# Kernel tuning notes

Hardware: AMD Instinct MI355X
Metric: run time of the kernel (lower is better)

The kernel has to match this reference:

```python
import jax, jax.numpy as jnp
import numpy as np

N_HEADS, D_MODEL, D_HEAD, N_CTX = 16, 2048, 128, 2048
BATCH, SEQ = 2, 2048
ATTN_SCALE = float(np.sqrt(D_HEAD))
IGNORE = -100000.0


def setup_inputs() -> dict:
    key = jax.random.key(0)
    ks = jax.random.split(key, 6)
    init = 0.02
    return {
        "residual": jax.random.normal(ks[0], (BATCH, SEQ, D_MODEL), dtype=jnp.float32),
        "x": jax.random.normal(ks[1], (BATCH, SEQ, D_MODEL), dtype=jnp.float32),
        "W_Q": jax.random.normal(ks[2], (N_HEADS, D_MODEL, D_HEAD), dtype=jnp.float32) * init,
        "W_K": jax.random.normal(ks[3], (N_HEADS, D_MODEL, D_HEAD), dtype=jnp.float32) * init,
        "W_V": jax.random.normal(ks[4], (N_HEADS, D_MODEL, D_HEAD), dtype=jnp.float32) * init,
        "W_O": jax.random.normal(ks[5], (N_HEADS, D_HEAD, D_MODEL), dtype=jnp.float32) * init,
        "b_Q": jnp.zeros((N_HEADS, D_HEAD), dtype=jnp.float32),
        "b_K": jnp.zeros((N_HEADS, D_HEAD), dtype=jnp.float32),
        "b_V": jnp.zeros((N_HEADS, D_HEAD), dtype=jnp.float32),
        "b_O": jnp.zeros((D_MODEL,), dtype=jnp.float32),
    }


def reference(residual, x, W_Q, W_K, W_V, W_O, b_Q, b_K, b_V, b_O):
    # use_split_qkv_input=False: QKV all read from residual
    q = jnp.einsum('bpm,hmd->bphd', residual, W_Q) + b_Q  # [b, pos, h, d_head]
    k = jnp.einsum('bpm,hmd->bphd', residual, W_K) + b_K
    v = jnp.einsum('bpm,hmd->bphd', residual, W_V) + b_V
    attn_scores = jnp.einsum('bqhd,bkhd->bhqk', q, k) / ATTN_SCALE  # [b, h, q, k]
    key_len = attn_scores.shape[-1]
    mask = jnp.tril(jnp.ones((key_len, key_len), dtype=bool))  # causal mask [q, k]
    attn_scores = jnp.where(mask, attn_scores, IGNORE)
    pattern = jax.nn.softmax(attn_scores, axis=-1)
    z = jnp.einsum('bkhd,bhqk->bqhd', v, pattern)
    out = jnp.einsum('bphd,hdm->bpm', z, W_O) + b_O
    return (residual, out)
```

## Files before the change

### kernel.cpp

```cpp
#include <hip/hip_runtime.h>
#include <hip/hip_bf16.h>

typedef __attribute__((ext_vector_type(8))) short bf16x8;
typedef __attribute__((ext_vector_type(4))) float f32x4;

#define N_HEADS 16
#define D_MODEL 2048
#define D_HEAD  128
#define SEQ     2048
#define BATCH   2
#define HD      (N_HEADS * D_HEAD)
#define QSCALE  0.08838834764831845f

__device__ inline __hip_bfloat16 to_bf16(float v) { return __float2bfloat16(v); }
__device__ inline __hip_bfloat16 to_bf16(__hip_bfloat16 v) { return v; }

typedef __attribute__((address_space(3))) unsigned lds_u32_t;
typedef __attribute__((address_space(1))) unsigned glb_u32_t;
__device__ inline void async16(void* l, const void* g) {
    __builtin_amdgcn_global_load_lds((const glb_u32_t*)g, (lds_u32_t*)l, 16, 0, 0);
}

__global__ __launch_bounds__(256) void cvt_dual(
    const float4* __restrict__ in, float4* __restrict__ o32,
    __hip_bfloat16* __restrict__ obf, long n4)
{
    for (long i = (long)blockIdx.x * blockDim.x + threadIdx.x; i < n4;
         i += (long)gridDim.x * blockDim.x) {
        float4 v = in[i];
        o32[i] = v;
        union { __hip_bfloat16 b[4]; uint2 u; } p;
        p.b[0] = __float2bfloat16(v.x);
        p.b[1] = __float2bfloat16(v.y);
        p.b[2] = __float2bfloat16(v.z);
        p.b[3] = __float2bfloat16(v.w);
        *(uint2*)(obf + 4 * i) = p.u;
    }
}

template <typename Tin>
__global__ __launch_bounds__(256) void transpose_to_bf16(
    const Tin* __restrict__ in, __hip_bfloat16* __restrict__ out,
    int R, int C, long in_rs, long in_bs, long out_bs)
{
    __shared__ Tin tile[64][65];
    const Tin* src = in + (long)blockIdx.z * in_bs;
    __hip_bfloat16* dst = out + (long)blockIdx.z * out_bs;
    const int c0 = blockIdx.x * 64, r0 = blockIdx.y * 64;
    const int t = threadIdx.x;
    const int tr = t >> 4;
    const int tc = (t & 15) * 4;
#pragma unroll
    for (int i = 0; i < 4; i++) {
        int r = tr + i * 16;
#pragma unroll
        for (int j = 0; j < 4; j++)
            tile[r][tc + j] = src[(long)(r0 + r) * in_rs + c0 + tc + j];
    }
    __syncthreads();
#pragma unroll
    for (int i = 0; i < 4; i++) {
        int c = tr + i * 16;
#pragma unroll
        for (int j = 0; j < 4; j++)
            dst[(long)(c0 + c) * R + r0 + tc + j] = to_bf16(tile[tc + j][c]);
    }
}

__device__ inline void store_out(__hip_bfloat16* p, float v) { *p = __float2bfloat16(v); }
__device__ inline void store_out(float* p, float v) { *p = v; }

template <typename OutT>
__global__ __launch_bounds__(256) void gemm_qkv(
    const __hip_bfloat16* __restrict__ A,
    const __hip_bfloat16* __restrict__ WTbase,
    const float* __restrict__ bQ, const float* bK, const float* bV,
    OutT* __restrict__ Cbase,
    int M, int N, int K, long wstride, long cstride, float scale0)
{
    __shared__ __align__(16) __hip_bfloat16 As[128 * 32];
    __shared__ __align__(16) __hip_bfloat16 Bs[128 * 32];
    const int z = blockIdx.z;
    const __hip_bfloat16* Bt = WTbase + (long)z * wstride;
    const float* bias = (z == 0) ? bQ : ((z == 1) ? bK : bV);
    OutT* C = Cbase + (long)z * cstride;
    const float outscale = (z == 0) ? scale0 : 1.0f;

    const int tid = threadIdx.x;
    const int lane = tid & 63, wave = tid >> 6;
    const int l15 = lane & 15, quad = lane >> 4;
    const int wr = wave >> 1, wc = wave & 1;
    const int m0 = blockIdx.y * 128, n0 = blockIdx.x * 128;

    const short* Ap = (const short*)A;
    const short* Bp = (const short*)Bt;

    f32x4 acc[4][4] = {};

    for (int k0 = 0; k0 < K; k0 += 32) {
        __syncthreads();
#pragma unroll
        for (int i = 0; i < 2; i++) {
            int e = i * 256 + tid;
            int row = e >> 2, ch = e & 3;
            async16((char*)As + (i * 256 + wave * 64) * 16,
                    Ap + (long)(m0 + row) * K + k0 + ch * 8);
            async16((char*)Bs + (i * 256 + wave * 64) * 16,
                    Bp + (long)(n0 + row) * K + k0 + ch * 8);
        }
        __syncthreads();

        bf16x8 af[4], bfr[4];
#pragma unroll
        for (int t = 0; t < 4; t++) {
            af[t]  = *(const bf16x8*)((const short*)As + (wr * 64 + t * 16 + l15) * 32 + quad * 8);
            bfr[t] = *(const bf16x8*)((const short*)Bs + (wc * 64 + t * 16 + l15) * 32 + quad * 8);
        }
#pragma unroll
        for (int i = 0; i < 4; i++)
#pragma unroll
            for (int j = 0; j < 4; j++)
                acc[i][j] = __builtin_amdgcn_mfma_f32_16x16x32_bf16(af[i], bfr[j], acc[i][j], 0, 0, 0);
    }

    const int mw = m0 + wr * 64, nw = n0 + wc * 64;
#pragma unroll
    for (int i = 0; i < 4; i++) {
#pragma unroll
        for (int j = 0; j < 4; j++) {
            int n = nw + j * 16 + l15;
            float bv = bias[n];
#pragma unroll
            for (int r = 0; r < 4; r++) {
                int m = mw + i * 16 + quad * 4 + r;
                store_out(&C[(long)m * N + n], (acc[i][j][r] + bv) * outscale);
            }
        }
    }
}

template <typename OutT>
__global__ __launch_bounds__(512, 2) void gemm256(
    const __hip_bfloat16* __restrict__ A,
    const __hip_bfloat16* __restrict__ WTbase,
    const float* __restrict__ bQ, const float* bK, const float* bV,
    OutT* __restrict__ Cbase,
    int N, int K, long wstride, long cstride, float scale0,
    int nx, int ny)
{
    __shared__ __align__(16) short lds[2][4][128 * 64];

    const int tid = threadIdx.x;
    const int lane = tid & 63;
    const int wave = tid >> 6;
    const int l15 = lane & 15, quad = lane >> 4, l7 = lane & 7;
    const int wm = wave >> 2, wn = wave & 3;

    const int nwg = gridDim.x;
    const int orig = blockIdx.x;
    const int wg = (orig & 7) * (nwg >> 3) + (orig >> 3);
    const int nxy = nx * ny;
    const int z = wg / nxy;
    const int rem = wg - z * nxy;
    const int by = rem / nx;
    const int bx = rem - by * nx;
    const int m0 = by * 256, n0 = bx * 256;

    const short* Ap = (const short*)A;
    const short* Bp = (const short*)WTbase + (long)z * wstride;

    const int r0 = tid >> 3;
    const int c0 = (tid & 7) ^ (r0 & 7);
    const int r1 = 64 + r0;

    auto stageA = [&](int bf, int reg, int kt) {
        char* base = (char*)&lds[bf][reg][0];
        const short* g = Ap + (long)(m0 + reg * 128) * K + kt * 64;
        async16(base + wave * 1024,        g + (long)r0 * K + c0 * 8);
        async16(base + 8192 + wave * 1024, g + (long)r1 * K + c0 * 8);
    };
    auto stageB = [&](int bf, int reg, int kt) {
        char* base = (char*)&lds[bf][2 + reg][0];
        const short* g = Bp + (long)(n0 + reg * 128) * K + kt * 64;
        async16(base + wave * 1024,        g + (long)r0 * K + c0 * 8);
        async16(base + 8192 + wave * 1024, g + (long)r1 * K + c0 * 8);
    };

    const int NT = K >> 6;

    stageA(0, 0, 0); stageA(0, 1, 0); stageB(0, 0, 0); stageB(0, 1, 0);
    stageB(1, 0, 1); stageB(1, 1, 1); stageA(1, 0, 1);
    asm volatile("s_waitcnt vmcnt(6)" ::: "memory");
    __builtin_amdgcn_s_barrier();

    f32x4 acc[8][4] = {};
    const int br0 = (wn & 1) * 64;

#pragma unroll 2
    for (int u = 0; u < NT; ++u) {
        asm volatile("" ::: "memory");
        const int bf = u & 1, bo = bf ^ 1;
        const short* la = &lds[bf][wm][0];
        const short* lb = &lds[bf][2 + (wn >> 1)][0];

        bf16x8 a[4][2], b0[2][2], b1[2][2];

#pragma unroll
        for (int fm = 0; fm < 4; fm++)
#pragma unroll
            for (int kk = 0; kk < 2; kk++)
                a[fm][kk] = *(const bf16x8*)(la + (fm * 16 + l15) * 64
                                             + (((kk * 4 + quad) ^ l7) * 8));
#pragma unroll
        for (int fn = 0; fn < 2; fn++)
#pragma unroll
            for (int kk = 0; kk < 2; kk++)
                b0[fn][kk] = *(const bf16x8*)(lb + (br0 + fn * 16 + l15) * 64
                                              + (((kk * 4 + quad) ^ l7) * 8));
        if (u + 1 < NT) stageA(bo, 1, u + 1);
        __builtin_amdgcn_s_barrier();
        asm volatile("s_waitcnt lgkmcnt(0)" ::: "memory");
        __builtin_amdgcn_sched_barrier(0);
        __builtin_amdgcn_s_setprio(1);
#pragma unroll
        for (int fm = 0; fm < 4; fm++)
#pragma unroll
            for (int fn = 0; fn < 2; fn++)
#pragma unroll
                for (int kk = 0; kk < 2; kk++)
                    acc[fm][fn] = __builtin_amdgcn_mfma_f32_16x16x32_bf16(
                        a[fm][kk], b0[fn][kk], acc[fm][fn], 0, 0, 0);
        __builtin_amdgcn_s_setprio(0);
        __builtin_amdgcn_s_barrier();

#pragma unroll
        for (int fn = 0; fn < 2; fn++)
#pragma unroll
            for (int kk = 0; kk < 2; kk++)
                b1[fn][kk] = *(const bf16x8*)(lb + (br0 + 32 + fn * 16 + l15) * 64
                                              + (((kk * 4 + quad) ^ l7) * 8));
        if (u + 2 < NT) stageB(bf, 0, u + 2);
        __builtin_amdgcn_s_barrier();
        asm volatile("s_waitcnt lgkmcnt(0)" ::: "memory");
        __builtin_amdgcn_sched_barrier(0);
        __builtin_amdgcn_s_setprio(1);
#pragma unroll
        for (int fm = 0; fm < 4; fm++)
#pragma unroll
            for (int fn = 0; fn < 2; fn++)
#pragma unroll
                for (int kk = 0; kk < 2; kk++)
                    acc[fm][2 + fn] = __builtin_amdgcn_mfma_f32_16x16x32_bf16(
                        a[fm][kk], b1[fn][kk], acc[fm][2 + fn], 0, 0, 0);
        __builtin_amdgcn_s_setprio(0);
        __builtin_amdgcn_s_barrier();

#pragma unroll
        for (int fm = 0; fm < 4; fm++)
#pragma unroll
            for (int kk = 0; kk < 2; kk++)
                a[fm][kk] = *(const bf16x8*)(la + (64 + fm * 16 + l15) * 64
                                             + (((kk * 4 + quad) ^ l7) * 8));
        if (u + 2 < NT) stageB(bf, 1, u + 2);
        __builtin_amdgcn_s_barrier();
        asm volatile("s_waitcnt lgkmcnt(0)" ::: "memory");
        __builtin_amdgcn_sched_barrier(0);
        __builtin_amdgcn_s_setprio(1);
#pragma unroll
        for (int fm = 0; fm < 4; fm++)
#pragma unroll
            for (int fn = 0; fn < 2; fn++)
#pragma unroll
                for (int kk = 0; kk < 2; kk++)
                    acc[4 + fm][2 + fn] = __builtin_amdgcn_mfma_f32_16x16x32_bf16(
                        a[fm][kk], b1[fn][kk], acc[4 + fm][2 + fn], 0, 0, 0);
        __builtin_amdgcn_s_setprio(0);
        __builtin_amdgcn_s_barrier();

        if (u + 2 < NT) stageA(bf, 0, u + 2);
        __builtin_amdgcn_s_barrier();
        __builtin_amdgcn_s_setprio(1);
#pragma unroll
        for (int fm = 0; fm < 4; fm++)
#pragma unroll
            for (int fn = 0; fn < 2; fn++)
#pragma unroll
                for (int kk = 0; kk < 2; kk++)
                    acc[4 + fm][fn] = __builtin_amdgcn_mfma_f32_16x16x32_bf16(
                        a[fm][kk], b0[fn][kk], acc[4 + fm][fn], 0, 0, 0);
        __builtin_amdgcn_s_setprio(0);
        if (u + 2 < NT) {
            asm volatile("s_waitcnt vmcnt(6)" ::: "memory");
        } else if (u + 1 < NT) {
            asm volatile("s_waitcnt vmcnt(0)" ::: "memory");
        }
        __builtin_amdgcn_s_barrier();
    }

    const float* bias = (z == 0) ? bQ : ((z == 1) ? bK : bV);
    OutT* C = Cbase + (long)z * cstride;
    const float outscale = (z == 0) ? scale0 : 1.0f;
#pragma unroll
    for (int mi = 0; mi < 8; mi++) {
#pragma unroll
        for (int nj = 0; nj < 4; nj++) {
            const int n = n0 + wn * 64 + nj * 16 + l15;
            const float bv = bias[n];
#pragma unroll
            for (int r = 0; r < 4; r++) {
                const int m = m0 + wm * 128 + mi * 16 + quad * 4 + r;
                store_out(&C[(long)m * N + n], (acc[mi][nj][r] + bv) * outscale);
            }
        }
    }
}

__global__ __launch_bounds__(256) void attn_fused(
    const __hip_bfloat16* Q,
    const __hip_bfloat16* __restrict__ Kin,
    const __hip_bfloat16* __restrict__ Vt,
    __hip_bfloat16* Z)
{
    __shared__ __align__(16) __hip_bfloat16 Ks[64 * 128];
    __shared__ __align__(16) __hip_bfloat16 Vs[128 * 64];
    __shared__ __align__(16) __hip_bfloat16 pbuf[4][32 * 72];

    const int tid = threadIdx.x;
    const int lane = tid & 63, wave = tid >> 6;
    const int l15 = lane & 15, quad = lane >> 4;

    const int g0id = blockIdx.x;
    const int qt = (g0id < 256) ? (15 - (g0id & 15)) : (g0id & 15);
    const int hb = ((g0id >> 4) & 15) + ((g0id >> 8) << 4);
    const int b = hb >> 4, h = hb & 15;

    const short* Qp = (const short*)Q;
    const short* Kp = (const short*)Kin;
    const short* Vp = (const short*)Vt;

    bf16x8 aq[2][4];
#pragma unroll
    for (int g = 0; g < 2; g++)
#pragma unroll
        for (int ks = 0; ks < 4; ks++)
            aq[g][ks] = *(const bf16x8*)(Qp + (long)(b * SEQ + qt * 128 + g * 64 + wave * 16 + l15) * HD
                                         + h * D_HEAD + ks * 32 + quad * 8);

    f32x4 o[2][8] = {};
    float lsum[2][4] = {};

    const short* pw = (const short*)pbuf[wave];

    const int ktiles = 2 * qt + 2;
    for (int kt = 0; kt < ktiles; kt++) {
        const int kb = kt * 64;
        __syncthreads();
#pragma unroll
        for (int i = 0; i < 4; i++) {
            int e = i * 256 + tid;
            int row = e >> 4, cc = (e & 15) ^ (row & 7);
            async16((char*)Ks + (size_t)e * 16,
                    Kp + (long)(b * SEQ + kb + row) * HD + h * D_HEAD + cc * 8);
        }
#pragma unroll
        for (int i = 0; i < 4; i++) {
            int e = i * 256 + tid;
            int row = e >> 3, cc = (e & 7) ^ (row & 7);
            async16((char*)Vs + (size_t)e * 16,
                    Vp + ((long)(b * N_HEADS + h) * D_HEAD + row) * SEQ + kb + cc * 8);
        }
        __syncthreads();

        f32x4 s[2][4] = {};
#pragma unroll
        for (int nt = 0; nt < 4; nt++)
#pragma unroll
            for (int ks = 0; ks < 4; ks++) {
                bf16x8 bk = *(const bf16x8*)((const short*)Ks + (nt * 16 + l15) * 128
                                             + (((ks * 4 + quad) ^ (l15 & 7)) * 8));
                s[0][nt] = __builtin_amdgcn_mfma_f32_16x16x32_bf16(aq[0][ks], bk, s[0][nt], 0, 0, 0);
                s[1][nt] = __builtin_amdgcn_mfma_f32_16x16x32_bf16(aq[1][ks], bk, s[1][nt], 0, 0, 0);
            }

#pragma unroll
        for (int g = 0; g < 2; g++) {
            if (kt >= 2 * qt + g) {
                bool full = kt > 2 * qt + g;
#pragma unroll
                for (int nt = 0; nt < 4; nt++)
#pragma unroll
                    for (int r = 0; r < 4; r++) {
                        int qq = wave * 16 + quad * 4 + r;
                        int kk = nt * 16 + l15;
                        if (full || kk > qq) s[g][nt][r] = -100000.0f;
                    }
            }
        }

#pragma unroll
        for (int g = 0; g < 2; g++) {
#pragma unroll
            for (int nt = 0; nt < 4; nt++)
#pragma unroll
                for (int r = 0; r < 4; r++) {
                    float p = __expf(s[g][nt][r]);
                    s[g][nt][r] = p;
                    lsum[g][r] += p;
                    pbuf[wave][(g * 16 + quad * 4 + r) * 72 + nt * 16 + l15] = __float2bfloat16(p);
                }
        }

#pragma unroll
        for (int ks2 = 0; ks2 < 2; ks2++) {
            bf16x8 ap0 = *(const bf16x8*)(pw + (0  + l15) * 72 + ks2 * 32 + quad * 8);
            bf16x8 ap1 = *(const bf16x8*)(pw + (16 + l15) * 72 + ks2 * 32 + quad * 8);
#pragma unroll
            for (int tj = 0; tj < 8; tj++) {
                bf16x8 bv = *(const bf16x8*)((const short*)Vs + (tj * 16 + l15) * 64
                                             + (((ks2 * 4 + quad) ^ (l15 & 7)) * 8));
                o[0][tj] = __builtin_amdgcn_mfma_f32_16x16x32_bf16(ap0, bv, o[0][tj], 0, 0, 0);
                o[1][tj] = __builtin_amdgcn_mfma_f32_16x16x32_bf16(ap1, bv, o[1][tj], 0, 0, 0);
            }
        }
    }

#pragma unroll
    for (int g = 0; g < 2; g++) {
        float inv[4];
#pragma unroll
        for (int r = 0; r < 4; r++) {
            float v = lsum[g][r];
#pragma unroll
            for (int ofs = 1; ofs < 16; ofs <<= 1)
                v += __shfl_xor(v, ofs, 64);
            inv[r] = 1.0f / v;
        }
#pragma unroll
        for (int tj = 0; tj < 8; tj++)
#pragma unroll
            for (int r = 0; r < 4; r++) {
                long q = b * SEQ + qt * 128 + g * 64 + wave * 16 + quad * 4 + r;
                Z[q * HD + h * D_HEAD + tj * 16 + l15] = __float2bfloat16(o[g][tj][r] * inv[r]);
            }
    }
}

extern "C" void kernel_launch(void* const* d_in, const int* in_sizes, int n_in,
                              void* d_out, int out_size, void* d_ws, size_t ws_size,
                              hipStream_t stream)
{
    const float* residual = (const float*)d_in[0];
    const float* W_Q = (const float*)d_in[2];
    const float* W_K = (const float*)d_in[3];
    const float* W_V = (const float*)d_in[4];
    const float* W_O = (const float*)d_in[5];
    const float* b_Q = (const float*)d_in[6];
    const float* b_K = (const float*)d_in[7];
    const float* b_V = (const float*)d_in[8];
    const float* b_O = (const float*)d_in[9];
    float* out = (float*)d_out;

    const long TOK = (long)BATCH * SEQ;
    const long TD = TOK * D_MODEL;
    const long WSZ = (long)D_MODEL * D_MODEL;
    char* ws = (char*)d_ws;
    __hip_bfloat16* Qb = (__hip_bfloat16*)(ws);
    __hip_bfloat16* Kb = (__hip_bfloat16*)(ws + TD * 2);
    __hip_bfloat16* Vb = (__hip_bfloat16*)(ws + TD * 4);
    __hip_bfloat16* Rb = (__hip_bfloat16*)(ws + TD * 6);
    __hip_bfloat16* Vt = Rb;
    __hip_bfloat16* WT = (__hip_bfloat16*)(ws + TD * 8);
    __hip_bfloat16* Zb = Qb;

    const size_t NEED_BIG = (size_t)TD * 8 + (size_t)WSZ * 2 * 3;
    const bool big = ws_size >= NEED_BIG;

    dim3 tB(256);

    cvt_dual<<<2048, tB, 0, stream>>>((const float4*)residual, (float4*)out, Rb, TD / 4);

    dim3 gridWqkv(D_HEAD / 64, D_MODEL / 64, N_HEADS);
    const float* Wqkv[3] = {W_Q, W_K, W_V};
    const float* bqkv[3] = {b_Q, b_K, b_V};

    if (big) {
        for (int z = 0; z < 3; z++)
            transpose_to_bf16<float><<<gridWqkv, tB, 0, stream>>>(
                Wqkv[z], WT + (long)z * WSZ, D_MODEL, D_HEAD,
                D_HEAD, (long)D_MODEL * D_HEAD, (long)D_HEAD * D_MODEL);
        gemm256<__hip_bfloat16><<<dim3(384), dim3(512), 0, stream>>>(
            Rb, WT, b_Q, b_K, b_V, Qb, D_MODEL, D_MODEL,
            WSZ, TD, QSCALE, D_MODEL / 256, (int)(TOK / 256));
    } else {
        dim3 gridG(D_MODEL / 128, (int)(TOK / 128), 1);
        for (int z = 0; z < 3; z++) {
            transpose_to_bf16<float><<<gridWqkv, tB, 0, stream>>>(
                Wqkv[z], WT, D_MODEL, D_HEAD,
                D_HEAD, (long)D_MODEL * D_HEAD, (long)D_HEAD * D_MODEL);
            gemm_qkv<__hip_bfloat16><<<gridG, tB, 0, stream>>>(
                Rb, WT, bqkv[z], bqkv[z], bqkv[z], Qb + (long)z * TD,
                (int)TOK, D_MODEL, D_MODEL, 0, 0, z == 0 ? QSCALE : 1.0f);
        }
    }

    dim3 gridVt(D_HEAD / 64, SEQ / 64, N_HEADS);
    for (int b = 0; b < BATCH; b++) {
        transpose_to_bf16<__hip_bfloat16><<<gridVt, tB, 0, stream>>>(
            Vb + (long)b * SEQ * D_MODEL, Vt + (long)b * N_HEADS * D_HEAD * SEQ,
            SEQ, D_HEAD, (long)D_MODEL, (long)D_HEAD, (long)D_HEAD * SEQ);
    }

    attn_fused<<<dim3(512), dim3(256), 0, stream>>>(Qb, Kb, Vt, Zb);

    dim3 gridWo(D_MODEL / 64, D_MODEL / 64, 1);
    transpose_to_bf16<float><<<gridWo, tB, 0, stream>>>(
        W_O, WT, D_MODEL, D_MODEL, (long)D_MODEL, 0, 0);
    gemm256<float><<<dim3(128), dim3(512), 0, stream>>>(
        Zb, WT, b_O, b_O, b_O, out + TD, D_MODEL, D_MODEL,
        0, 0, 1.0f, D_MODEL / 256, (int)(TOK / 256));
}
```

Baseline: 473.6 us.

## Shrink GEMM tile to 256x128 to double block count and fill CUs

```diff
diff --git a/kernel.cpp b/kernel.cpp
--- a/kernel.cpp
+++ b/kernel.cpp
@@ -140,7 +140,7 @@
 }
 
 template <typename OutT>
-__global__ __launch_bounds__(512, 2) void gemm256(
+__global__ __launch_bounds__(512, 2) void gemm256x128(
     const __hip_bfloat16* __restrict__ A,
     const __hip_bfloat16* __restrict__ WTbase,
     const float* __restrict__ bQ, const float* bK, const float* bV,
@@ -148,13 +148,13 @@
     int N, int K, long wstride, long cstride, float scale0,
     int nx, int ny)
 {
-    __shared__ __align__(16) short lds[2][4][128 * 64];
+    __shared__ __align__(16) short lds[2][3][128 * 64];
 
     const int tid = threadIdx.x;
     const int lane = tid & 63;
     const int wave = tid >> 6;
     const int l15 = lane & 15, quad = lane >> 4, l7 = lane & 7;
-    const int wm = wave >> 2, wn = wave & 3;
+    const int wm = wave >> 1, wn = wave & 1;
 
     const int nwg = gridDim.x;
     const int orig = blockIdx.x;
@@ -164,7 +164,7 @@
     const int rem = wg - z * nxy;
     const int by = rem / nx;
     const int bx = rem - by * nx;
-    const int m0 = by * 256, n0 = bx * 256;
+    const int m0 = by * 256, n0 = bx * 128;
 
     const short* Ap = (const short*)A;
     const short* Bp = (const short*)WTbase + (long)z * wstride;
@@ -179,29 +179,30 @@
         async16(base + wave * 1024,        g + (long)r0 * K + c0 * 8);
         async16(base + 8192 + wave * 1024, g + (long)r1 * K + c0 * 8);
     };
-    auto stageB = [&](int bf, int reg, int kt) {
-        char* base = (char*)&lds[bf][2 + reg][0];
-        const short* g = Bp + (long)(n0 + reg * 128) * K + kt * 64;
+    auto stageB = [&](int bf, int kt) {
+        char* base = (char*)&lds[bf][2][0];
+        const short* g = Bp + (long)(n0 + 0) * K + kt * 64;
         async16(base + wave * 1024,        g + (long)r0 * K + c0 * 8);
         async16(base + 8192 + wave * 1024, g + (long)r1 * K + c0 * 8);
     };
 
     const int NT = K >> 6;
 
-    stageA(0, 0, 0); stageA(0, 1, 0); stageB(0, 0, 0); stageB(0, 1, 0);
-    stageB(1, 0, 1); stageB(1, 1, 1); stageA(1, 0, 1);
-    asm volatile("s_waitcnt vmcnt(6)" ::: "memory");
+    stageA(0, 0, 0); stageA(0, 1, 0); stageB(0, 0);
+    stageA(1, 0, 1); stageA(1, 1, 1);
+    asm volatile("s_waitcnt vmcnt(4)" ::: "memory");
     __builtin_amdgcn_s_barrier();
 
-    f32x4 acc[8][4] = {};
-    const int br0 = (wn & 1) * 64;
+    f32x4 acc[4][4] = {};
+    const int ar0 = (wm & 1) * 64;
+    const int br0 = wn * 64;
 
 #pragma unroll 2
     for (int u = 0; u < NT; ++u) {
         asm volatile("" ::: "memory");
         const int bf = u & 1, bo = bf ^ 1;
-        const short* la = &lds[bf][wm][0];
-        const short* lb = &lds[bf][2 + (wn >> 1)][0];
+        const short* la = &lds[bf][wm >> 1][0];
+        const short* lb = &lds[bf][2][0];
 
         bf16x8 a[4][2], b0[2][2], b1[2][2];
 
@@ -209,7 +210,7 @@
         for (int fm = 0; fm < 4; fm++)
 #pragma unroll
             for (int kk = 0; kk < 2; kk++)
-                a[fm][kk] = *(const bf16x8*)(la + (fm * 16 + l15) * 64
+                a[fm][kk] = *(const bf16x8*)(la + (ar0 + fm * 16 + l15) * 64
                                              + (((kk * 4 + quad) ^ l7) * 8));
 #pragma unroll
         for (int fn = 0; fn < 2; fn++)
@@ -217,7 +218,7 @@
             for (int kk = 0; kk < 2; kk++)
                 b0[fn][kk] = *(const bf16x8*)(lb + (br0 + fn * 16 + l15) * 64
                                               + (((kk * 4 + quad) ^ l7) * 8));
-        if (u + 1 < NT) stageA(bo, 1, u + 1);
+        if (u + 1 < NT) stageB(bo, u + 1);
         __builtin_amdgcn_s_barrier();
         asm volatile("s_waitcnt lgkmcnt(0)" ::: "memory");
         __builtin_amdgcn_sched_barrier(0);
@@ -239,7 +240,7 @@
             for (int kk = 0; kk < 2; kk++)
                 b1[fn][kk] = *(const bf16x8*)(lb + (br0 + 32 + fn * 16 + l15) * 64
                                               + (((kk * 4 + quad) ^ l7) * 8));
-        if (u + 2 < NT) stageB(bf, 0, u + 2);
+        if (u + 2 < NT) { stageA(bf, 0, u + 2); stageA(bf, 1, u + 2); }
         __builtin_amdgcn_s_barrier();
         asm volatile("s_waitcnt lgkmcnt(0)" ::: "memory");
         __builtin_amdgcn_sched_barrier(0);
@@ -253,44 +254,8 @@
                     acc[fm][2 + fn] = __builtin_amdgcn_mfma_f32_16x16x32_bf16(
                         a[fm][kk], b1[fn][kk], acc[fm][2 + fn], 0, 0, 0);
         __builtin_amdgcn_s_setprio(0);
-        __builtin_amdgcn_s_barrier();
-
-#pragma unroll
-        for (int fm = 0; fm < 4; fm++)
-#pragma unroll
-            for (int kk = 0; kk < 2; kk++)
-                a[fm][kk] = *(const bf16x8*)(la + (64 + fm * 16 + l15) * 64
-                                             + (((kk * 4 + quad) ^ l7) * 8));
-        if (u + 2 < NT) stageB(bf, 1, u + 2);
-        __builtin_amdgcn_s_barrier();
-        asm volatile("s_waitcnt lgkmcnt(0)" ::: "memory");
-        __builtin_amdgcn_sched_barrier(0);
-        __builtin_amdgcn_s_setprio(1);
-#pragma unroll
-        for (int fm = 0; fm < 4; fm++)
-#pragma unroll
-            for (int fn = 0; fn < 2; fn++)
-#pragma unroll
-                for (int kk = 0; kk < 2; kk++)
-                    acc[4 + fm][2 + fn] = __builtin_amdgcn_mfma_f32_16x16x32_bf16(
-                        a[fm][kk], b1[fn][kk], acc[4 + fm][2 + fn], 0, 0, 0);
-        __builtin_amdgcn_s_setprio(0);
-        __builtin_amdgcn_s_barrier();
-
-        if (u + 2 < NT) stageA(bf, 0, u + 2);
-        __builtin_amdgcn_s_barrier();
-        __builtin_amdgcn_s_setprio(1);
-#pragma unroll
-        for (int fm = 0; fm < 4; fm++)
-#pragma unroll
-            for (int fn = 0; fn < 2; fn++)
-#pragma unroll
-                for (int kk = 0; kk < 2; kk++)
-                    acc[4 + fm][fn] = __builtin_amdgcn_mfma_f32_16x16x32_bf16(
-                        a[fm][kk], b0[fn][kk], acc[4 + fm][fn], 0, 0, 0);
-        __builtin_amdgcn_s_setprio(0);
         if (u + 2 < NT) {
-            asm volatile("s_waitcnt vmcnt(6)" ::: "memory");
+            asm volatile("s_waitcnt vmcnt(4)" ::: "memory");
         } else if (u + 1 < NT) {
             asm volatile("s_waitcnt vmcnt(0)" ::: "memory");
         }
@@ -301,14 +266,14 @@
     OutT* C = Cbase + (long)z * cstride;
     const float outscale = (z == 0) ? scale0 : 1.0f;
 #pragma unroll
-    for (int mi = 0; mi < 8; mi++) {
+    for (int mi = 0; mi < 4; mi++) {
 #pragma unroll
         for (int nj = 0; nj < 4; nj++) {
             const int n = n0 + wn * 64 + nj * 16 + l15;
             const float bv = bias[n];
 #pragma unroll
             for (int r = 0; r < 4; r++) {
-                const int m = m0 + wm * 128 + mi * 16 + quad * 4 + r;
+                const int m = m0 + wm * 64 + mi * 16 + quad * 4 + r;
                 store_out(&C[(long)m * N + n], (acc[mi][nj][r] + bv) * outscale);
             }
         }
@@ -488,9 +453,9 @@
             transpose_to_bf16<float><<<gridWqkv, tB, 0, stream>>>(
                 Wqkv[z], WT + (long)z * WSZ, D_MODEL, D_HEAD,
                 D_HEAD, (long)D_MODEL * D_HEAD, (long)D_HEAD * D_MODEL);
-        gemm256<__hip_bfloat16><<<dim3(384), dim3(512), 0, stream>>>(
+        gemm256x128<__hip_bfloat16><<<dim3(768), dim3(512), 0, stream>>>(
             Rb, WT, b_Q, b_K, b_V, Qb, D_MODEL, D_MODEL,
-            WSZ, TD, QSCALE, D_MODEL / 256, (int)(TOK / 256));
+            WSZ, TD, QSCALE, D_MODEL / 128, (int)(TOK / 256));
     } else {
         dim3 gridG(D_MODEL / 128, (int)(TOK / 128), 1);
         for (int z = 0; z < 3; z++) {
@@ -515,7 +480,13 @@
     dim3 gridWo(D_MODEL / 64, D_MODEL / 64, 1);
     transpose_to_bf16<float><<<gridWo, tB, 0, stream>>>(
         W_O, WT, D_MODEL, D_MODEL, (long)D_MODEL, 0, 0);
-    gemm256<float><<<dim3(128), dim3(512), 0, stream>>>(
-        Zb, WT, b_O, b_O, b_O, out + TD, D_MODEL, D_MODEL,
-        0, 0, 1.0f, D_MODEL / 256, (int)(TOK / 256));
-}
+    if (big) {
+        gemm256x128<float><<<dim3(256), dim3(512), 0, stream>>>(
+            Zb, WT, b_O, b_O, b_O, out + TD, D_MODEL, D_MODEL,
+            0, 0, 1.0f, D_MODEL / 128, (int)(TOK / 256));
+    } else {
+        dim3 gridO(D_MODEL / 128, (int)(TOK / 128), 1);
+        gemm_qkv<float><<<gridO, tB, 0, stream>>>(
+            Zb, WT, b_O, b_O, b_O, out + TD, (int)TOK, D_MODEL, D_MODEL, 0, 0, 1.0f);
+    }
+}
```

New measurement: 445.7 us. 1.06x faster.
